# Optimization experiments

Measured on AMD Instinct MI355X. Metric: run time of the kernel, lower is better.

Reference implementation:

```python
import jax, jax.numpy as jnp
import numpy as np

DIM = 2048
N_HEADS = 16
N_KV_HEADS = 4
ROPE_BASE = 10000.0
QK_GAIN_INIT = 1.0
B, T = 4, 2048


def setup_inputs() -> dict:
    key = jax.random.key(0)
    ks = jax.random.split(key, 5)
    head_dim = DIM // N_HEADS
    kv_dim = N_KV_HEADS * head_dim
    x = jax.random.normal(ks[0], (B, T, DIM), dtype=jnp.float32)
    wq = jax.random.normal(ks[1], (DIM, DIM), dtype=jnp.float32) * 0.02
    wk = jax.random.normal(ks[2], (kv_dim, DIM), dtype=jnp.float32) * 0.02
    wv = jax.random.normal(ks[3], (kv_dim, DIM), dtype=jnp.float32) * 0.02
    wo = jax.random.normal(ks[4], (DIM, DIM), dtype=jnp.float32) * 0.02
    q_gain = jnp.full((N_HEADS,), QK_GAIN_INIT, dtype=jnp.float32)
    k_gain = jnp.full((N_KV_HEADS,), QK_GAIN_INIT, dtype=jnp.float32)
    return {"x": x, "wq": wq, "wk": wk, "wv": wv, "wo": wo,
            "q_gain": q_gain, "k_gain": k_gain}


def _rope_tables(T, head_dim, dtype):
    # inv_freq over even indices, freqs = outer(t, inv_freq) -> [T, head_dim//2]
    inv_freq = ROPE_BASE ** (-jnp.arange(0, head_dim, 2, dtype=jnp.float32) / head_dim)
    freqs = jnp.arange(T, dtype=jnp.float32)[:, None] * inv_freq[None, :]
    return jnp.cos(freqs).astype(dtype), jnp.sin(freqs).astype(dtype)


def _apply_rotary(x, cos, sin):
    # x: [..., T, head_dim]; cos/sin: [T, head_dim//2] broadcast over leading dims
    half = x.shape[-1] // 2
    x1, x2 = x[..., :half], x[..., half:]
    return jnp.concatenate((x1 * cos + x2 * sin, -x1 * sin + x2 * cos), axis=-1)


def reference(x, wq, wk, wv, wo, q_gain, k_gain):
    Bx, Tx, C = x.shape
    H, KV = N_HEADS, N_KV_HEADS
    D = C // H
    G = H // KV  # query groups per kv head

    q = (x @ wq.T).reshape(Bx, Tx, H, D)    # [B,T,H,D]
    k = (x @ wk.T).reshape(Bx, Tx, KV, D)   # [B,T,KV,D]
    v = (x @ wv.T).reshape(Bx, Tx, KV, D)

    q = q * q_gain[None, None, :, None]
    k = k * k_gain[None, None, :, None]

    cos, sin = _rope_tables(Tx, D, x.dtype)
    q = _apply_rotary(q.transpose(0, 2, 1, 3), cos, sin)  # [B,H,T,D]
    k = _apply_rotary(k.transpose(0, 2, 1, 3), cos, sin)  # [B,KV,T,D]
    v = v.transpose(0, 2, 1, 3)                            # [B,KV,T,D]

    # GQA without materializing repeated k/v: group query heads per kv head
    q = q.reshape(Bx, KV, G, Tx, D)
    scale = 1.0 / jnp.sqrt(jnp.array(D, dtype=x.dtype))
    scores = jnp.einsum('bkgtd,bksd->bkgts', q, k) * scale  # [B,KV,G,T,T]
    causal = jnp.tril(jnp.ones((Tx, Tx), dtype=bool))
    scores = jnp.where(causal, scores, jnp.finfo(scores.dtype).min)
    attn = jax.nn.softmax(scores, axis=-1)
    y = jnp.einsum('bkgts,bksd->bkgtd', attn, v)            # [B,KV,G,T,D]
    y = y.reshape(Bx, H, Tx, D).transpose(0, 2, 1, 3).reshape(Bx, Tx, C)
    return y @ wo.T
```

## Files before the change

kernel.cpp:

```cpp
#include <hip/hip_runtime.h>
#include <hip/hip_bf16.h>

typedef __bf16 bf16x8 __attribute__((ext_vector_type(8)));
typedef float f32x4 __attribute__((ext_vector_type(4)));

#define DIMC 2048
#define HD   128
#define NH   16
#define NKV  4
#define BSZ  4
#define TSZ  2048
#define MROWS (BSZ * TSZ)
#define NQKV  (DIMC + 2 * NKV * HD)


__device__ __forceinline__ void async_copy16(const void* g, void* l) {
  __builtin_amdgcn_global_load_lds(
      (const __attribute__((address_space(1))) void*)g,
      (__attribute__((address_space(3))) void*)l, 16, 0, 0);
}


__global__ void cvt_all(const float* __restrict__ x, const float* __restrict__ wq,
                        const float* __restrict__ wk, const float* __restrict__ wv,
                        const float* __restrict__ wo, __hip_bfloat16* __restrict__ dst) {
  const long n0 = (long)MROWS * DIMC;
  const long n1 = n0 + (long)DIMC * DIMC;
  const long n2 = n1 + (long)NKV * HD * DIMC;
  const long n3 = n2 + (long)NKV * HD * DIMC;
  long i = ((long)blockIdx.x * blockDim.x + threadIdx.x) * 4;
  const float* src; long off;
  if (i < n0)      { src = x;  off = i; }
  else if (i < n1) { src = wq; off = i - n0; }
  else if (i < n2) { src = wk; off = i - n1; }
  else if (i < n3) { src = wv; off = i - n2; }
  else             { src = wo; off = i - n3; }
  float4 v = *(const float4*)(src + off);
  union { __hip_bfloat16 b[4]; short4 s; } u;
  u.b[0] = __float2bfloat16(v.x);
  u.b[1] = __float2bfloat16(v.y);
  u.b[2] = __float2bfloat16(v.z);
  u.b[3] = __float2bfloat16(v.w);
  *(short4*)(dst + i) = u.s;
}


__global__ void rope_tab(float* __restrict__ ct, float* __restrict__ st) {
  int idx = blockIdx.x * blockDim.x + threadIdx.x;
  int d = idx & 63, t = idx >> 6;
  float inv = powf(10000.0f, -(float)d * (1.0f / 64.0f));
  float f = (float)t * inv;
  ct[idx] = cosf(f);
  st[idx] = sinf(f);
}


template <int NF>
__device__ __forceinline__ void load_frags(const __hip_bfloat16* p, int rbase,
                                           int quad, int l7, int l15,
                                           bf16x8 fr[NF][2]) {
#pragma unroll
  for (int i = 0; i < NF; i++) {
    const int r = rbase + i * 16 + l15;
#pragma unroll
    for (int kk = 0; kk < 2; kk++)
      fr[i][kk] = *(const bf16x8*)&p[r * 64 + (((kk << 2) + quad) ^ l7) * 8];
  }
}

template <int NBF, int NW>
__device__ __forceinline__ void mq(f32x4 (*acc)[NBF], const bf16x8 a[4][2],
                                   const bf16x8 (*b)[2], int mb, int nb) {
#pragma unroll
  for (int kk = 0; kk < 2; kk++)
#pragma unroll
    for (int mi = 0; mi < 4; mi++)
#pragma unroll
      for (int ni = 0; ni < NW; ni++)
        acc[mb + mi][nb + ni] = __builtin_amdgcn_mfma_f32_16x16x32_bf16(
            a[mi][kk], b[nb + ni][kk], acc[mb + mi][nb + ni], 0, 0, 0);
}

template <int OUT_BF16, int NBF>
__global__ __launch_bounds__(512, 2) void gemm256_bt(
    const __hip_bfloat16* __restrict__ A, const __hip_bfloat16* __restrict__ Bw,
    void* __restrict__ Cv, int M, int N, int K) {
  constexpr int BN = NBF * 64;
  __shared__ __align__(16) __hip_bfloat16 lsA[2][16384];
  __shared__ __align__(16) __hip_bfloat16 lsB[2][BN * 64];
  const int tid = threadIdx.x;
  const int w = tid >> 6, lane = tid & 63;
  const int quad = lane >> 4, l15 = lane & 15, l7 = lane & 7;
  const int wr = w >> 2, wc = w & 3;
  const int wrow = wr * 128, wcol = wc * (NBF * 16);
  const int wbase = w * 512;

  const int nwg = gridDim.x * gridDim.y;
  const int bid = blockIdx.y * gridDim.x + blockIdx.x;
  const int sw = (bid & 7) * (nwg >> 3) + (bid >> 3);
  const int m0 = (sw / gridDim.x) * 256, n0 = (sw % gridDim.x) * BN;

  const int NTt = K >> 6;

  const __hip_bfloat16 *gA0, *gB0;
  {
    const int r0 = tid >> 3, c0 = ((tid & 7) ^ (r0 & 7)) * 8;
    gA0 = A + (long)(m0 + r0) * K + c0;
    gB0 = Bw + (long)(n0 + r0) * K + c0;
  }

  auto stA = [&](int t2, int rp) {
    if (t2 >= NTt) return;
    async_copy16(gA0 + (long)rp * 64 * K + (t2 << 6),
                 &lsA[t2 & 1][rp * 4096 + wbase]);
  };
  auto stB = [&](int t2, int rp) {
    if (t2 >= NTt) return;
    async_copy16(gB0 + (long)rp * 64 * K + (t2 << 6),
                 &lsB[t2 & 1][rp * 4096 + wbase]);
  };

  f32x4 acc[8][NBF] = {};
  bf16x8 a[4][2], b[NBF][2];

#pragma unroll
  for (int rp = 0; rp < NBF; rp++) stB(0, rp);
#pragma unroll
  for (int rp = 0; rp < 4; rp++) stA(0, rp);
#pragma unroll
  for (int rp = 0; rp < NBF; rp++) stB(1, rp);
  stA(1, 0); stA(1, 1);
  if constexpr (NBF == 3) asm volatile("s_waitcnt vmcnt(5)" ::: "memory");
  else                    asm volatile("s_waitcnt vmcnt(6)" ::: "memory");
  __builtin_amdgcn_s_barrier();

  for (int t = 0; t < NTt; t++) {
    const __hip_bfloat16* pA = lsA[t & 1];
    const __hip_bfloat16* pB = lsB[t & 1];

    load_frags<4>(pA, wrow, quad, l7, l15, a);
    load_frags<NBF>(pB, wcol, quad, l7, l15, b);
    stA(t + 1, 2); stA(t + 1, 3);
    asm volatile("s_waitcnt lgkmcnt(8)" ::: "memory");
    __builtin_amdgcn_s_barrier();
    asm volatile("s_waitcnt lgkmcnt(0)" ::: "memory");
    __builtin_amdgcn_s_setprio(1);
    mq<NBF, 2>(acc, a, b, 0, 0);
    __builtin_amdgcn_s_setprio(0);
    __builtin_amdgcn_s_barrier();

    stB(t + 2, 0); stB(t + 2, 1);
    __builtin_amdgcn_s_barrier();
    __builtin_amdgcn_s_setprio(1);
    mq<NBF, NBF - 2>(acc, a, b, 0, 2);
    __builtin_amdgcn_s_setprio(0);
    __builtin_amdgcn_s_barrier();

    load_frags<4>(pA, wrow + 64, quad, l7, l15, a);
#pragma unroll
    for (int rp = 2; rp < NBF; rp++) stB(t + 2, rp);
    __builtin_amdgcn_s_barrier();
    asm volatile("s_waitcnt lgkmcnt(0)" ::: "memory");
    __builtin_amdgcn_s_setprio(1);
    mq<NBF, 2>(acc, a, b, 4, 0);
    __builtin_amdgcn_s_setprio(0);
    __builtin_amdgcn_s_barrier();

    stA(t + 2, 0); stA(t + 2, 1);
    __builtin_amdgcn_s_barrier();
    __builtin_amdgcn_s_setprio(1);
    mq<NBF, NBF - 2>(acc, a, b, 4, 2);
    __builtin_amdgcn_s_setprio(0);
    if (t < NTt - 3) {
      if constexpr (NBF == 3) asm volatile("s_waitcnt vmcnt(5)" ::: "memory");
      else                    asm volatile("s_waitcnt vmcnt(6)" ::: "memory");
    } else {
      asm volatile("s_waitcnt vmcnt(0)" ::: "memory");
    }
    __builtin_amdgcn_s_barrier();
  }

#pragma unroll
  for (int mi = 0; mi < 8; mi++) {
#pragma unroll
    for (int r = 0; r < 4; r++) {
      const long row = m0 + wrow + mi * 16 + quad * 4 + r;
      if (OUT_BF16) {
        __hip_bfloat16* Cb = (__hip_bfloat16*)Cv;
#pragma unroll
        for (int ni = 0; ni < NBF; ni++)
          Cb[row * N + n0 + wcol + ni * 16 + l15] = __float2bfloat16(acc[mi][ni][r]);
      } else {
        float* Cf = (float*)Cv;
#pragma unroll
        for (int ni = 0; ni < NBF; ni++)
          Cf[row * N + n0 + wcol + ni * 16 + l15] = acc[mi][ni][r];
      }
    }
  }
}


__global__ void rope_apply(const __hip_bfloat16* __restrict__ qkv,
                           const float* __restrict__ ct, const float* __restrict__ st,
                           const float* __restrict__ qg, const float* __restrict__ kg,
                           __hip_bfloat16* __restrict__ qr, __hip_bfloat16* __restrict__ kr) {
  const long QN = (long)BSZ * TSZ * NH * 64;
  long idx = (long)blockIdx.x * blockDim.x + threadIdx.x;
  if (idx < QN) {
    int d = idx & 63;
    int h = (int)((idx >> 6) & 15);
    long bt = idx >> 10;
    int t = (int)(bt & (TSZ - 1));
    long base = bt * NQKV + h * HD + d;
    float x1 = __bfloat162float(qkv[base]);
    float x2 = __bfloat162float(qkv[base + 64]);
    float c = ct[t * 64 + d], s = st[t * 64 + d];
    float g = qg[h] * 0.08838834764831845f * 1.4426950408889634f;
    long ob = ((bt >> 11) * NH + h) * ((long)TSZ * HD) + (long)t * HD + d;
    qr[ob]      = __float2bfloat16((x1 * c + x2 * s) * g);
    qr[ob + 64] = __float2bfloat16((-x1 * s + x2 * c) * g);
  } else {
    long j = idx - QN;
    int d = (int)(j & 63);
    int kv = (int)((j >> 6) & 3);
    long bt = j >> 8;
    int t = (int)(bt & (TSZ - 1));
    long base = bt * NQKV + DIMC + kv * HD + d;
    float x1 = __bfloat162float(qkv[base]);
    float x2 = __bfloat162float(qkv[base + 64]);
    float c = ct[t * 64 + d], s = st[t * 64 + d];
    float g = kg[kv];
    long ob = ((bt >> 11) * NKV + kv) * ((long)TSZ * HD) + (long)t * HD + d;
    kr[ob]      = __float2bfloat16((x1 * c + x2 * s) * g);
    kr[ob + 64] = __float2bfloat16((-x1 * s + x2 * c) * g);
  }
}


__global__ void vtrans(const __hip_bfloat16* __restrict__ qkv, __hip_bfloat16* __restrict__ vt) {
  __shared__ __hip_bfloat16 tile[64][65];
  const int bkv = blockIdx.z;
  const int b = bkv >> 2, kv = bkv & 3;
  const int t0 = blockIdx.y * 64, d0 = blockIdx.x * 64;
  const int tx = threadIdx.x, ty = threadIdx.y;
#pragma unroll
  for (int i = 0; i < 8; i++) {
    int t = ty + i * 8;
    tile[t][tx] = qkv[(long)(b * TSZ + t0 + t) * NQKV + DIMC + NKV * HD + kv * HD + d0 + tx];
  }
  __syncthreads();
#pragma unroll
  for (int i = 0; i < 8; i++) {
    int d = ty + i * 8;
    vt[((long)((b * NKV + kv) * HD + d0 + d)) * TSZ + t0 + tx] = tile[tx][d];
  }
}


__global__ __launch_bounds__(256, 2) void attn(
    const __hip_bfloat16* __restrict__ Q, const __hip_bfloat16* __restrict__ Kr,
    const __hip_bfloat16* __restrict__ Vt, __hip_bfloat16* __restrict__ Y) {
  __shared__ __align__(16) __hip_bfloat16 lds_v[2][64 * 128];
  __shared__ __align__(16) __hip_bfloat16 lds_k[64 * 128];
  __shared__ __align__(16) __hip_bfloat16 lds_p[4][32 * 64];
  const int qpair = blockIdx.x, bh = blockIdx.y;
  const int b = bh >> 4, h = bh & 15, kv = h >> 2;
  const int tid = threadIdx.x, wave = tid >> 6, lane = tid & 63;
  const int quad = lane >> 4, l15 = lane & 15, l7 = lane & 7;
  const __hip_bfloat16* Kp = Kr + (long)(b * NKV + kv) * TSZ * HD;
  const __hip_bfloat16* Vp = Vt + (long)(b * NKV + kv) * HD * TSZ;

  union { short u[8]; bf16x8 v; } ones;
#pragma unroll
  for (int i = 0; i < 8; i++) ones.u[i] = 0x3F80;

  auto stageK = [&](int j) {
#pragma unroll
    for (int i = 0; i < 4; i++) {
      int p = (i * 4 + wave) * 64 + lane;
      int row = p >> 4;
      int gc = (p & 15) ^ (row & 7);
      async_copy16(Kp + (long)j * 8192 + row * 128 + gc * 8, &lds_k[(i * 4 + wave) * 512]);
    }
  };
  auto stageV = [&](int j, int buf) {
#pragma unroll
    for (int i = 0; i < 4; i++) {
      int p = (i * 4 + wave) * 64 + lane;
      int d = p >> 3;
      int gc = (p & 7) ^ (d & 7);
      async_copy16(Vp + (long)d * TSZ + j * 64 + gc * 8, &lds_v[buf][(i * 4 + wave) * 512]);
    }
  };

  for (int half = 0; half < 2; half++) {
    const int qi = half ? (15 - qpair) : qpair;
    const __hip_bfloat16* Qp = Q + ((long)(b * NH + h) * TSZ + qi * 128 + wave * 32) * HD;
    bf16x8 aq[2][4];
#pragma unroll
    for (int ni = 0; ni < 2; ni++)
#pragma unroll
      for (int kk = 0; kk < 4; kk++)
        aq[ni][kk] = *(const bf16x8*)&Qp[(ni * 16 + l15) * HD + kk * 32 + quad * 8];

    f32x4 o[2][8] = {};
    f32x4 osum[2] = {};
    const int njt = 2 * qi + 2;

    stageV(0, 0);
    stageK(0);
    for (int j = 0; j < njt; j++) {
      __syncthreads();
      if (j + 1 < njt) stageV(j + 1, (j + 1) & 1);

      f32x4 s[4][2] = {};
#pragma unroll
      for (int kk = 0; kk < 4; kk++) {
        bf16x8 bk[4];
#pragma unroll
        for (int mi = 0; mi < 4; mi++)
          bk[mi] = *(const bf16x8*)&lds_k[(mi * 16 + l15) * 128 + ((kk * 4 + quad) ^ l7) * 8];
#pragma unroll
        for (int mi = 0; mi < 4; mi++)
#pragma unroll
          for (int ni = 0; ni < 2; ni++)
            s[mi][ni] = __builtin_amdgcn_mfma_f32_16x16x32_bf16(bk[mi], aq[ni][kk], s[mi][ni], 0, 0, 0);
      }

      const bool diag = (j >= 2 * qi);
#pragma unroll
      for (int mi = 0; mi < 4; mi++) {
#pragma unroll
        for (int ni = 0; ni < 2; ni++) {
          f32x4 p4;
          if (diag) {
            int qrow = qi * 128 + wave * 32 + ni * 16 + l15;
            int kbase = j * 64 + mi * 16 + quad * 4;
#pragma unroll
            for (int r = 0; r < 4; r++)
              p4[r] = (kbase + r <= qrow) ? exp2f(s[mi][ni][r]) : 0.f;
          } else {
#pragma unroll
            for (int r = 0; r < 4; r++) p4[r] = exp2f(s[mi][ni][r]);
          }
          const int c = mi * 4 + quad;
          const int addr = (ni * 16 + l15) * 64 + (((c >> 1) ^ l7) * 2 + (c & 1)) * 4;
          union { __hip_bfloat162 h2[2]; uint2 u; } pk;
          pk.h2[0] = __float22bfloat162_rn(float2{p4[0], p4[1]});
          pk.h2[1] = __float22bfloat162_rn(float2{p4[2], p4[3]});
          *(uint2*)&lds_p[wave][addr] = pk.u;
        }
      }

      asm volatile("s_barrier" ::: "memory");
      if (j + 1 < njt) stageK(j + 1);
      asm volatile("s_waitcnt lgkmcnt(0)" ::: "memory");

      const __hip_bfloat16* lv = lds_v[j & 1];
#pragma unroll
      for (int kk = 0; kk < 2; kk++) {
        bf16x8 ap[2];
#pragma unroll
        for (int mi = 0; mi < 2; mi++)
          ap[mi] = *(const bf16x8*)&lds_p[wave][(mi * 16 + l15) * 64 + ((kk * 4 + quad) ^ l7) * 8];
#pragma unroll
        for (int mi = 0; mi < 2; mi++)
          osum[mi] = __builtin_amdgcn_mfma_f32_16x16x32_bf16(ap[mi], ones.v, osum[mi], 0, 0, 0);
#pragma unroll
        for (int nd = 0; nd < 8; nd++) {
          bf16x8 bv = *(const bf16x8*)&lv[(nd * 16 + l15) * 64 + ((kk * 4 + quad) ^ l7) * 8];
#pragma unroll
          for (int mi = 0; mi < 2; mi++)
            o[mi][nd] = __builtin_amdgcn_mfma_f32_16x16x32_bf16(ap[mi], bv, o[mi][nd], 0, 0, 0);
        }
      }
    }

    const long yb0 = (long)b * TSZ + qi * 128 + wave * 32;
#pragma unroll
    for (int mi = 0; mi < 2; mi++) {
#pragma unroll
      for (int r = 0; r < 4; r++) {
        float inv = 1.0f / osum[mi][r];
        long row = yb0 + mi * 16 + quad * 4 + r;
#pragma unroll
        for (int nd = 0; nd < 8; nd++)
          Y[row * DIMC + h * HD + nd * 16 + l15] = __float2bfloat16(o[mi][nd][r] * inv);
      }
    }
    __syncthreads();
  }
}


extern "C" void kernel_launch(void* const* d_in, const int* in_sizes, int n_in,
                              void* d_out, int out_size, void* d_ws, size_t ws_size,
                              hipStream_t stream) {
  const float* x  = (const float*)d_in[0];
  const float* wq = (const float*)d_in[1];
  const float* wk = (const float*)d_in[2];
  const float* wv = (const float*)d_in[3];
  const float* wo = (const float*)d_in[4];
  const float* qg = (const float*)d_in[5];
  const float* kg = (const float*)d_in[6];

  char* ws = (char*)d_ws;
  size_t off = 0;
  auto alloc = [&](size_t bytes) {
    char* p = ws + off;
    off += (bytes + 255) & ~(size_t)255;
    return p;
  };
  __hip_bfloat16* xb    = (__hip_bfloat16*)alloc((size_t)MROWS * DIMC * 2);
  __hip_bfloat16* wqkvb = (__hip_bfloat16*)alloc((size_t)NQKV * DIMC * 2);
  __hip_bfloat16* wob   = (__hip_bfloat16*)alloc((size_t)DIMC * DIMC * 2);
  __hip_bfloat16* qkv   = (__hip_bfloat16*)alloc((size_t)MROWS * NQKV * 2);
  __hip_bfloat16* qr    = (__hip_bfloat16*)alloc((size_t)MROWS * DIMC * 2);
  __hip_bfloat16* kr    = (__hip_bfloat16*)alloc((size_t)BSZ * NKV * TSZ * HD * 2);
  __hip_bfloat16* vt    = (__hip_bfloat16*)alloc((size_t)BSZ * NKV * TSZ * HD * 2);
  float* ct = (float*)alloc((size_t)TSZ * 64 * 4);
  float* st = (float*)alloc((size_t)TSZ * 64 * 4);
  __hip_bfloat16* yb = xb;

  const long NCVT = (long)MROWS * DIMC + (long)DIMC * DIMC * 2 + (long)NKV * HD * DIMC * 2;
  cvt_all<<<NCVT / 1024, 256, 0, stream>>>(x, wq, wk, wv, wo, xb);
  rope_tab<<<TSZ * 64 / 256, 256, 0, stream>>>(ct, st);

  gemm256_bt<1, 3><<<dim3(NQKV / 192, MROWS / 256), 512, 0, stream>>>(xb, wqkvb, qkv, MROWS, NQKV, DIMC);

  const long QN = (long)BSZ * TSZ * NH * 64;
  const long KN = (long)BSZ * TSZ * NKV * 64;
  rope_apply<<<(QN + KN) / 256, 256, 0, stream>>>(qkv, ct, st, qg, kg, qr, kr);
  vtrans<<<dim3(HD / 64, TSZ / 64, BSZ * NKV), dim3(64, 8), 0, stream>>>(qkv, vt);

  attn<<<dim3(8, BSZ * NH), 256, 0, stream>>>(qr, kr, vt, yb);

  gemm256_bt<0, 4><<<dim3(DIMC / 256, MROWS / 256), 512, 0, stream>>>(yb, wob, d_out, MROWS, DIMC, DIMC);
}
```

Before: 439.7 us.

## Rewrite attention with 32x32 MFMA, register-resident P and 256-row query tiles

```diff
diff --git a/kernel.cpp b/kernel.cpp
--- a/kernel.cpp
+++ b/kernel.cpp
@@ -3,6 +3,7 @@
 
 typedef __bf16 bf16x8 __attribute__((ext_vector_type(8)));
 typedef float f32x4 __attribute__((ext_vector_type(4)));
+typedef float f32x16 __attribute__((ext_vector_type(16)));
 
 #define DIMC 2048
 #define HD   128
@@ -258,22 +259,19 @@
 }
 
 
-__global__ __launch_bounds__(256, 2) void attn(
+__global__ __launch_bounds__(256, 1) void attn(
     const __hip_bfloat16* __restrict__ Q, const __hip_bfloat16* __restrict__ Kr,
     const __hip_bfloat16* __restrict__ Vt, __hip_bfloat16* __restrict__ Y) {
-  __shared__ __align__(16) __hip_bfloat16 lds_v[2][64 * 128];
   __shared__ __align__(16) __hip_bfloat16 lds_k[64 * 128];
-  __shared__ __align__(16) __hip_bfloat16 lds_p[4][32 * 64];
-  const int qpair = blockIdx.x, bh = blockIdx.y;
+  __shared__ __align__(16) __hip_bfloat16 lds_v[2][128 * 64];
+  const int bid = blockIdx.x;
+  const int qi = 7 - (bid >> 6);
+  const int bh = bid & 63;
   const int b = bh >> 4, h = bh & 15, kv = h >> 2;
   const int tid = threadIdx.x, wave = tid >> 6, lane = tid & 63;
-  const int quad = lane >> 4, l15 = lane & 15, l7 = lane & 7;
+  const int hi = lane >> 5, l31 = lane & 31, l7 = lane & 7;
   const __hip_bfloat16* Kp = Kr + (long)(b * NKV + kv) * TSZ * HD;
   const __hip_bfloat16* Vp = Vt + (long)(b * NKV + kv) * HD * TSZ;
-
-  union { short u[8]; bf16x8 v; } ones;
-#pragma unroll
-  for (int i = 0; i < 8; i++) ones.u[i] = 0x3F80;
 
   auto stageK = [&](int j) {
 #pragma unroll
@@ -294,102 +292,122 @@
     }
   };
 
-  for (int half = 0; half < 2; half++) {
-    const int qi = half ? (15 - qpair) : qpair;
-    const __hip_bfloat16* Qp = Q + ((long)(b * NH + h) * TSZ + qi * 128 + wave * 32) * HD;
-    bf16x8 aq[2][4];
-#pragma unroll
-    for (int ni = 0; ni < 2; ni++)
-#pragma unroll
-      for (int kk = 0; kk < 4; kk++)
-        aq[ni][kk] = *(const bf16x8*)&Qp[(ni * 16 + l15) * HD + kk * 32 + quad * 8];
-
-    f32x4 o[2][8] = {};
-    f32x4 osum[2] = {};
-    const int njt = 2 * qi + 2;
-
-    stageV(0, 0);
-    stageK(0);
-    for (int j = 0; j < njt; j++) {
-      __syncthreads();
-      if (j + 1 < njt) stageV(j + 1, (j + 1) & 1);
-
-      f32x4 s[4][2] = {};
-#pragma unroll
-      for (int kk = 0; kk < 4; kk++) {
-        bf16x8 bk[4];
-#pragma unroll
-        for (int mi = 0; mi < 4; mi++)
-          bk[mi] = *(const bf16x8*)&lds_k[(mi * 16 + l15) * 128 + ((kk * 4 + quad) ^ l7) * 8];
-#pragma unroll
-        for (int mi = 0; mi < 4; mi++)
-#pragma unroll
-          for (int ni = 0; ni < 2; ni++)
-            s[mi][ni] = __builtin_amdgcn_mfma_f32_16x16x32_bf16(bk[mi], aq[ni][kk], s[mi][ni], 0, 0, 0);
-      }
-
-      const bool diag = (j >= 2 * qi);
-#pragma unroll
-      for (int mi = 0; mi < 4; mi++) {
+  const int qt0 = qi * 256 + wave * 64;
+  const int thr = 4 * qi + wave;
+  const int njt = 4 * qi + 4;
+
+  const __hip_bfloat16* Qp = Q + ((long)(b * NH + h) * TSZ + qt0) * HD;
+  bf16x8 qf[2][8];
+#pragma unroll
+  for (int ni = 0; ni < 2; ni++)
+#pragma unroll
+    for (int kk = 0; kk < 8; kk++)
+      qf[ni][kk] = *(const bf16x8*)&Qp[(ni * 32 + l31) * HD + kk * 16 + hi * 8];
+
+  f32x16 o[4][2] = {};
+  float osum[2] = {0.f, 0.f};
+
+  stageV(0, 0);
+  stageK(0);
+  for (int j = 0; j < njt; j++) {
+    __syncthreads();
+    if (j + 1 < njt) stageV(j + 1, (j + 1) & 1);
+
+    unsigned pw[4][2][4];
+    const bool active = (j <= thr);
+    if (active) {
+      const bool diag = (j == thr);
+#pragma unroll
+      for (int mi = 0; mi < 2; mi++) {
+        f32x16 s0 = {}, s1 = {};
+#pragma unroll
+        for (int kk = 0; kk < 8; kk++) {
+          bf16x8 kf = *(const bf16x8*)&lds_k[(mi * 32 + l31) * 128 + (((kk * 2 + hi) ^ l7)) * 8];
+          s0 = __builtin_amdgcn_mfma_f32_32x32x16_bf16(kf, qf[0][kk], s0, 0, 0, 0);
+          s1 = __builtin_amdgcn_mfma_f32_32x32x16_bf16(kf, qf[1][kk], s1, 0, 0, 0);
+        }
 #pragma unroll
         for (int ni = 0; ni < 2; ni++) {
-          f32x4 p4;
-          if (diag) {
-            int qrow = qi * 128 + wave * 32 + ni * 16 + l15;
-            int kbase = j * 64 + mi * 16 + quad * 4;
-#pragma unroll
-            for (int r = 0; r < 4; r++)
-              p4[r] = (kbase + r <= qrow) ? exp2f(s[mi][ni][r]) : 0.f;
-          } else {
-#pragma unroll
-            for (int r = 0; r < 4; r++) p4[r] = exp2f(s[mi][ni][r]);
+          const f32x16 sv = ni ? s1 : s0;
+          const int mode = diag ? (mi == ni ? 1 : (mi > ni ? 0 : 2)) : 2;
+          float p[16];
+#pragma unroll
+          for (int r = 0; r < 16; r++) {
+            if (mode == 2) {
+              p[r] = exp2f(sv[r]);
+            } else if (mode == 0) {
+              p[r] = 0.f;
+            } else {
+              int kl = mi * 32 + (r & 3) + 8 * (r >> 2) + 4 * hi;
+              int qr_ = ni * 32 + l31;
+              p[r] = (kl <= qr_) ? exp2f(sv[r]) : 0.f;
+            }
           }
-          const int c = mi * 4 + quad;
-          const int addr = (ni * 16 + l15) * 64 + (((c >> 1) ^ l7) * 2 + (c & 1)) * 4;
-          union { __hip_bfloat162 h2[2]; uint2 u; } pk;
-          pk.h2[0] = __float22bfloat162_rn(float2{p4[0], p4[1]});
-          pk.h2[1] = __float22bfloat162_rn(float2{p4[2], p4[3]});
-          *(uint2*)&lds_p[wave][addr] = pk.u;
+          float a0 = 0.f;
+#pragma unroll
+          for (int r = 0; r < 16; r++) a0 += p[r];
+          osum[ni] += a0;
+          unsigned u[8];
+#pragma unroll
+          for (int q = 0; q < 8; q++) {
+            __hip_bfloat162 t = __float22bfloat162_rn(float2{p[2 * q], p[2 * q + 1]});
+            u[q] = *(unsigned*)&t;
+          }
+#pragma unroll
+          for (int h2 = 0; h2 < 2; h2++) {
+            const int kk = mi * 2 + h2;
+            unsigned a_ = u[h2 * 4 + 0], b_ = u[h2 * 4 + 1];
+            unsigned c_ = u[h2 * 4 + 2], d_ = u[h2 * 4 + 3];
+            unsigned t1 = (unsigned)__shfl_xor((int)(hi ? a_ : c_), 32, 64);
+            unsigned t2 = (unsigned)__shfl_xor((int)(hi ? b_ : d_), 32, 64);
+            pw[kk][ni][0] = hi ? t1 : a_;
+            pw[kk][ni][1] = hi ? t2 : b_;
+            pw[kk][ni][2] = hi ? c_ : t1;
+            pw[kk][ni][3] = hi ? d_ : t2;
+          }
         }
       }
-
-      asm volatile("s_barrier" ::: "memory");
-      if (j + 1 < njt) stageK(j + 1);
-      asm volatile("s_waitcnt lgkmcnt(0)" ::: "memory");
-
+    }
+
+    asm volatile("s_barrier" ::: "memory");
+    if (j + 1 < njt) stageK(j + 1);
+
+    if (active) {
       const __hip_bfloat16* lv = lds_v[j & 1];
 #pragma unroll
-      for (int kk = 0; kk < 2; kk++) {
-        bf16x8 ap[2];
-#pragma unroll
-        for (int mi = 0; mi < 2; mi++)
-          ap[mi] = *(const bf16x8*)&lds_p[wave][(mi * 16 + l15) * 64 + ((kk * 4 + quad) ^ l7) * 8];
-#pragma unroll
-        for (int mi = 0; mi < 2; mi++)
-          osum[mi] = __builtin_amdgcn_mfma_f32_16x16x32_bf16(ap[mi], ones.v, osum[mi], 0, 0, 0);
-#pragma unroll
-        for (int nd = 0; nd < 8; nd++) {
-          bf16x8 bv = *(const bf16x8*)&lv[(nd * 16 + l15) * 64 + ((kk * 4 + quad) ^ l7) * 8];
-#pragma unroll
-          for (int mi = 0; mi < 2; mi++)
-            o[mi][nd] = __builtin_amdgcn_mfma_f32_16x16x32_bf16(ap[mi], bv, o[mi][nd], 0, 0, 0);
+      for (int kk = 0; kk < 4; kk++) {
+        bf16x8 pb0 = *(const bf16x8*)&pw[kk][0][0];
+        bf16x8 pb1 = *(const bf16x8*)&pw[kk][1][0];
+#pragma unroll
+        for (int md = 0; md < 4; md++) {
+          bf16x8 vf = *(const bf16x8*)&lv[(md * 32 + l31) * 64 + (((kk * 2 + hi) ^ l7)) * 8];
+          o[md][0] = __builtin_amdgcn_mfma_f32_32x32x16_bf16(vf, pb0, o[md][0], 0, 0, 0);
+          o[md][1] = __builtin_amdgcn_mfma_f32_32x32x16_bf16(vf, pb1, o[md][1], 0, 0, 0);
         }
       }
     }
-
-    const long yb0 = (long)b * TSZ + qi * 128 + wave * 32;
-#pragma unroll
-    for (int mi = 0; mi < 2; mi++) {
-#pragma unroll
-      for (int r = 0; r < 4; r++) {
-        float inv = 1.0f / osum[mi][r];
-        long row = yb0 + mi * 16 + quad * 4 + r;
-#pragma unroll
-        for (int nd = 0; nd < 8; nd++)
-          Y[row * DIMC + h * HD + nd * 16 + l15] = __float2bfloat16(o[mi][nd][r] * inv);
+  }
+
+  float inv[2];
+#pragma unroll
+  for (int ni = 0; ni < 2; ni++) {
+    float tot = osum[ni] + __shfl_xor(osum[ni], 32, 64);
+    inv[ni] = 1.0f / tot;
+  }
+#pragma unroll
+  for (int md = 0; md < 4; md++) {
+#pragma unroll
+    for (int ni = 0; ni < 2; ni++) {
+      const long row = (long)b * TSZ + qt0 + ni * 32 + l31;
+#pragma unroll
+      for (int rg = 0; rg < 4; rg++) {
+        union { __hip_bfloat16 bb[4]; uint2 u; } pk4;
+#pragma unroll
+        for (int c = 0; c < 4; c++)
+          pk4.bb[c] = __float2bfloat16(o[md][ni][rg * 4 + c] * inv[ni]);
+        *(uint2*)&Y[row * DIMC + h * HD + md * 32 + rg * 8 + hi * 4] = pk4.u;
       }
     }
-    __syncthreads();
   }
 }
 
@@ -434,7 +452,7 @@
   rope_apply<<<(QN + KN) / 256, 256, 0, stream>>>(qkv, ct, st, qg, kg, qr, kr);
   vtrans<<<dim3(HD / 64, TSZ / 64, BSZ * NKV), dim3(64, 8), 0, stream>>>(qkv, vt);
 
-  attn<<<dim3(8, BSZ * NH), 256, 0, stream>>>(qr, kr, vt, yb);
+  attn<<<dim3(512), 256, 0, stream>>>(qr, kr, vt, yb);
 
   gemm256_bt<0, 4><<<dim3(DIMC / 256, MROWS / 256), 512, 0, stream>>>(yb, wob, d_out, MROWS, DIMC, DIMC);
 }
```

After: 508.7 us. 15.7% more time.
